# Optimization experiments

Hardware: AMD Instinct MI355X
Metric: run time of the kernel (lower is better)

Reference implementation:

```python
import jax, jax.numpy as jnp
import numpy as np

N_NODES = 100000; N_EDGES = 1600000; B = 16
IN_CH = 32; HID = 32; H1 = 4; OUT_CH = 32; H2 = 4; EDGE_DIM = 16
GMM_HID = 128; NUM_MIX = 3; ACTION_DIM = 10
NEG_SLOPE = 0.2  # PyG GATv2Conv default negative_slope


def _glorot(key, shape):
    return jax.random.normal(key, shape, dtype=jnp.float32) * (1.0 / np.sqrt(shape[-1]))


def setup_inputs() -> dict:
    key = jax.random.key(0)
    ks = jax.random.split(key, 20)
    x = jax.random.normal(ks[0], (N_NODES, IN_CH), jnp.float32)
    edge_index = jax.random.randint(ks[1], (2, N_EDGES), 0, N_NODES, dtype=jnp.int64)
    edge_attr = jax.random.normal(ks[2], (N_EDGES, EDGE_DIM), jnp.float32)
    batch = jnp.sort(jax.random.randint(ks[3], (N_NODES,), 0, B, dtype=jnp.int64))
    d1 = H1 * HID; d2 = H2 * OUT_CH
    return dict(
        x=x, edge_index=edge_index, edge_attr=edge_attr, batch=batch,
        W1l=_glorot(ks[4], (d1, IN_CH)), b1l=jnp.zeros((d1,), jnp.float32),
        W1r=_glorot(ks[5], (d1, IN_CH)), b1r=jnp.zeros((d1,), jnp.float32),
        W1e=_glorot(ks[6], (d1, EDGE_DIM)), att1=_glorot(ks[7], (H1, HID)),
        bias1=jnp.zeros((d1,), jnp.float32),
        W2l=_glorot(ks[8], (d2, d1)), b2l=jnp.zeros((d2,), jnp.float32),
        W2r=_glorot(ks[9], (d2, d1)), b2r=jnp.zeros((d2,), jnp.float32),
        W2e=_glorot(ks[10], (d2, EDGE_DIM)), att2=_glorot(ks[11], (H2, OUT_CH)),
        bias2=jnp.zeros((d2,), jnp.float32),
        Wg1=_glorot(ks[12], (GMM_HID, d2)), bg1=jnp.zeros((GMM_HID,), jnp.float32),
        Wg2=_glorot(ks[13], (NUM_MIX * 5, GMM_HID)), bg2=jnp.zeros((NUM_MIX * 5,), jnp.float32),
        Wp=_glorot(ks[14], (ACTION_DIM, d2)), bp=jnp.zeros((ACTION_DIM,), jnp.float32),
    )


def _gatv2(x, src, dst, ea, Wl, bl, Wr, br, We, att, bias, heads, ch):
    """PyG GATv2Conv with edge_dim, concat=True, add_self_loops=True (fill='mean'), eval mode."""
    N = x.shape[0]
    E = ea.shape[0]
    # self-loop edge_attr = mean of incoming edge attrs per target node (fill_value='mean')
    attr_sum = jax.ops.segment_sum(ea, dst, num_segments=N)
    cnt = jax.ops.segment_sum(jnp.ones((E, 1), ea.dtype), dst, num_segments=N)
    loop_attr = attr_sum / jnp.maximum(cnt, 1.0)
    loop = jnp.arange(N, dtype=src.dtype)
    s = jnp.concatenate([src, loop])
    d = jnp.concatenate([dst, loop])
    eaf = jnp.concatenate([ea, loop_attr], axis=0)  # [E+N, edge_dim]
    xl = (x @ Wl.T + bl).reshape(N, heads, ch)  # source transform (messages)
    xr = (x @ Wr.T + br).reshape(N, heads, ch)  # target transform
    ee = (eaf @ We.T).reshape(-1, heads, ch)
    m = jax.nn.leaky_relu(xl[s] + xr[d] + ee, NEG_SLOPE)  # [E+N, H, C]
    logit = jnp.einsum('ehc,hc->eh', m, att)  # attention logits per edge/head
    # segment softmax over edges sharing a target node (every node has a self-loop)
    mx = jax.ops.segment_max(logit, d, num_segments=N)
    ex = jnp.exp(logit - mx[d])
    den = jax.ops.segment_sum(ex, d, num_segments=N)
    alpha = ex / den[d]
    out = jax.ops.segment_sum(alpha[..., None] * xl[s], d, num_segments=N)  # [N, H, C]
    return out.reshape(N, heads * ch) + bias


def reference(x, edge_index, edge_attr, batch,
              W1l, b1l, W1r, b1r, W1e, att1, bias1,
              W2l, b2l, W2r, b2r, W2e, att2, bias2,
              Wg1, bg1, Wg2, bg2, Wp, bp):
    src, dst = edge_index[0], edge_index[1]
    y = jax.nn.elu(_gatv2(x, src, dst, edge_attr, W1l, b1l, W1r, b1r, W1e, att1, bias1, H1, HID))
    # dropout is identity in eval mode
    y = _gatv2(y, src, dst, edge_attr, W2l, b2l, W2r, b2r, W2e, att2, bias2, H2, OUT_CH)
    # global_mean_pool over batch
    gsum = jax.ops.segment_sum(y, batch, num_segments=B)
    gcnt = jax.ops.segment_sum(jnp.ones((y.shape[0], 1), y.dtype), batch, num_segments=B)
    g = gsum / jnp.maximum(gcnt, 1.0)  # [B, H2*OUT_CH]
    gmm_params = jax.nn.relu(g @ Wg1.T + bg1) @ Wg2.T + bg2  # [B, 15]
    num_proposals_logits = g @ Wp.T + bp  # [B, 10]
    return jnp.concatenate([gmm_params, num_proposals_logits], axis=-1)  # [B, 25]
```

## Files before the change

### kernel.cpp

```cpp
#include <hip/hip_runtime.h>
#include <math.h>

#define N_NODES 100000
#define N_EDGES 1600000
#define EN_TOT  (N_EDGES + N_NODES)
#define BATCH   16
#define EDGE_DIM 16
#define NEG_SLOPE 0.2f
#define NB_SCAN 391
#define LOG2E 1.44269504f

typedef float v2f __attribute__((ext_vector_type(2)));

__device__ __forceinline__ int rfl(int v) { return __builtin_amdgcn_readfirstlane(v); }

__device__ __forceinline__ v2f fma2(v2f a, v2f b, v2f c) {
#if __has_builtin(__builtin_elementwise_fma)
    return __builtin_elementwise_fma(a, b, c);
#else
    v2f r; r.x = fmaf(a.x, b.x, c.x); r.y = fmaf(a.y, b.y, c.y); return r;
#endif
}

template<int CTRL>
__device__ __forceinline__ float dpp_add(float p) {
    int t = __builtin_amdgcn_update_dpp(0, __float_as_int(p), CTRL, 0xF, 0xF, true);
    return p + __int_as_float(t);
}
__device__ __forceinline__ float red16(float p) {
    p = dpp_add<0xB1>(p);
    p = dpp_add<0x4E>(p);
    p = dpp_add<0x141>(p);
    p = dpp_add<0x140>(p);
    return p;
}

__global__ void zero_kernel(float* __restrict__ p, long long n) {
    long long i = (long long)blockIdx.x * blockDim.x + threadIdx.x;
    long long stride = (long long)gridDim.x * blockDim.x;
    for (; i < n; i += stride) p[i] = 0.0f;
}

__global__ void count_deg(const int* __restrict__ dst, int* __restrict__ deg,
                          int* __restrict__ rank) {
    int e = blockIdx.x * 256 + threadIdx.x;
    if (e < N_EDGES) rank[e] = atomicAdd(&deg[dst[e]], 1);
}

__global__ __launch_bounds__(256) void scan1(const int* __restrict__ deg,
                                             int* __restrict__ incl, int* __restrict__ bsum) {
    __shared__ int s[256];
    int n = blockIdx.x * 256 + threadIdx.x;
    int v = (n < N_NODES) ? deg[n] + 1 : 0;
    s[threadIdx.x] = v;
    __syncthreads();
    for (int off = 1; off < 256; off <<= 1) {
        int t = (threadIdx.x >= off) ? s[threadIdx.x - off] : 0;
        __syncthreads();
        s[threadIdx.x] += t;
        __syncthreads();
    }
    if (n < N_NODES) incl[n] = s[threadIdx.x];
    if (threadIdx.x == 255) bsum[blockIdx.x] = s[255];
}

__global__ __launch_bounds__(512) void scan2(int* __restrict__ bsum) {
    __shared__ int s[512];
    int t = threadIdx.x;
    int v = (t < NB_SCAN) ? bsum[t] : 0;
    s[t] = v;
    __syncthreads();
    for (int off = 1; off < 512; off <<= 1) {
        int u = (t >= off) ? s[t - off] : 0;
        __syncthreads();
        s[t] += u;
        __syncthreads();
    }
    if (t < NB_SCAN) bsum[t] = s[t] - v;
}

__global__ void scan3(const int* __restrict__ incl, const int* __restrict__ deg,
                      const int* __restrict__ bsum, int* __restrict__ offs) {
    int n = blockIdx.x * 256 + threadIdx.x;
    if (n < N_NODES) offs[n] = incl[n] - (deg[n] + 1) + bsum[blockIdx.x];
    if (n == 0) offs[N_NODES] = EN_TOT;
}

__global__ void scatter(const int* __restrict__ src, const int* __restrict__ dst,
                        const int* __restrict__ offs, const int* __restrict__ rank,
                        int2* __restrict__ csr) {
    int e = blockIdx.x * 256 + threadIdx.x;
    if (e < N_EDGES) {
        csr[offs[dst[e]] + rank[e]] = make_int2(src[e], e);
    } else if (e < EN_TOT) {
        int n = e - N_EDGES;
        csr[offs[n + 1] - 1] = make_int2(n, N_EDGES + n);
    }
}

__global__ __launch_bounds__(256) void loopattr_csr(const int* __restrict__ offs,
                                                    const int2* __restrict__ csr,
                                                    const float* __restrict__ ea,
                                                    float* __restrict__ lattr) {
    int node = blockIdx.x * 4 + (threadIdx.x >> 6);
    if (node >= N_NODES) return;
    int lane = threadIdx.x & 63;
    int row = offs[node];
    int degn = offs[node + 1] - 1 - row;
    int k = lane & 15, grp = lane >> 4;
    float acc = 0.0f;
    for (int i = grp; i < degn; i += 4) {
        int eid = csr[row + i].y;
        acc += ea[(long long)eid * EDGE_DIM + k];
    }
    acc += __shfl_xor(acc, 16);
    acc += __shfl_xor(acc, 32);
    if (lane < 16) lattr[(long long)node * EDGE_DIM + k] = acc / fmaxf((float)degn, 1.0f);
}

template<int K>
__global__ __launch_bounds__(256) void dual_linear(
    const float* __restrict__ in,
    const float* __restrict__ Wl, const float* __restrict__ bl,
    const float* __restrict__ Wr, const float* __restrict__ br,
    float* __restrict__ outl, float* __restrict__ outr, int N)
{
    constexpr int ROWS = 32;
    constexpr int K4 = K / 4;
    __shared__ float4 srow[ROWS][K4];
    int t = threadIdx.x;
    int base = blockIdx.x * ROWS;
    {
        const float4* in4 = (const float4*)in;
        for (int i = t; i < ROWS * K4; i += 256) {
            int r = i / K4, k = i - r * K4;
            int n = base + r;
            srow[r][k] = (n < N) ? in4[(size_t)n * K4 + k] : make_float4(0.f, 0.f, 0.f, 0.f);
        }
    }
    __syncthreads();
    const float* W  = (t < 128) ? Wl : Wr;
    const float* bb = (t < 128) ? bl : br;
    float* outp     = (t < 128) ? outl : outr;
    int j = t & 127;
    float bj = bb[j];
    float acc[ROWS];
#pragma unroll
    for (int r = 0; r < ROWS; ++r) acc[r] = bj;
    const float4* W4 = (const float4*)(W + (size_t)j * K);
    for (int kk = 0; kk < K4; ++kk) {
        float4 w = W4[kk];
#pragma unroll
        for (int r = 0; r < ROWS; ++r) {
            float4 a = srow[r][kk];
            acc[r] = fmaf(a.x, w.x, acc[r]);
            acc[r] = fmaf(a.y, w.y, acc[r]);
            acc[r] = fmaf(a.z, w.z, acc[r]);
            acc[r] = fmaf(a.w, w.w, acc[r]);
        }
    }
    for (int r = 0; r < ROWS; ++r) {
        int n = base + r;
        if (n < N) outp[(long long)n * 128 + j] = acc[r];
    }
}

template<int DO_ELU>
__global__ __launch_bounds__(256) void gat_fused(
    const int* __restrict__ offs, const int2* __restrict__ csr,
    const float* __restrict__ ea, const float* __restrict__ lattr,
    const float* __restrict__ We, const float* __restrict__ att,
    const v2f* __restrict__ xl2, const v2f* __restrict__ xr2,
    const float* __restrict__ bias, float* __restrict__ y)
{
    int node = blockIdx.x * 4 + (threadIdx.x >> 6);
    if (node >= N_NODES) return;
    int lane = threadIdx.x & 63;
    int c = lane << 1;

    v2f we0[8], we1[8];
    {
        const v2f* Wa = (const v2f*)(We + (size_t)c * EDGE_DIM);
        const v2f* Wb = (const v2f*)(We + (size_t)(c + 1) * EDGE_DIM);
#pragma unroll
        for (int q = 0; q < 8; ++q) { we0[q] = Wa[q]; we1[q] = Wb[q]; }
    }
    float2 atv = ((const float2*)att)[lane];
    float att0 = atv.x * LOG2E, att1 = atv.y * LOG2E;
    const float THR = 8.0f * LOG2E;

    int row  = rfl(offs[node]);
    int rend = rfl(offs[node + 1]);
    int last = rend - 1;
    v2f xrv = xr2[(size_t)node * 64 + lane];

    float m = -INFINITY, d = 0.f, acc0 = 0.f, acc1 = 0.f;

    auto attr_ptr = [&](int eid) -> const float4* {
        return (const float4*)((eid < N_EDGES) ? ea + (size_t)eid * EDGE_DIM
                                               : lattr + (size_t)(eid - N_EDGES) * EDGE_DIM);
    };

    auto body = [&](float4 A0, float4 A1, float4 A2, float4 A3, v2f xls) {
        v2f a[8] = { {A0.x,A0.y},{A0.z,A0.w},{A1.x,A1.y},{A1.z,A1.w},
                     {A2.x,A2.y},{A2.z,A2.w},{A3.x,A3.y},{A3.z,A3.w} };
        v2f ee0 = {0.f,0.f}, ee1 = {0.f,0.f};
#pragma unroll
        for (int q = 0; q < 8; ++q) {
            ee0 = fma2(a[q], we0[q], ee0);
            ee1 = fma2(a[q], we1[q], ee1);
        }
        float v0 = xls.x + xrv.x + ee0.x + ee0.y;
        float v1 = xls.y + xrv.y + ee1.x + ee1.y;
        v0 = fmaxf(v0, NEG_SLOPE * v0);
        v1 = fmaxf(v1, NEG_SLOPE * v1);
        float pl = red16(fmaf(v0, att0, v1 * att1));
        if (pl - m > THR) { float r_ = exp2f(m - pl); d *= r_; acc0 *= r_; acc1 *= r_; m = pl; }
        float w = exp2f(pl - m);
        d += w;
        acc0 = fmaf(w, xls.x, acc0);
        acc1 = fmaf(w, xls.y, acc1);
    };

    int2 se_a = csr[row];
    int2 se_b = csr[min(row + 1, last)];
    int2 se_c = csr[min(row + 2, last)];
    int2 se_d = csr[min(row + 3, last)];

    const float4* apA = attr_ptr(se_a.y);
    float4 Aa0 = apA[0], Aa1 = apA[1], Aa2 = apA[2], Aa3 = apA[3];
    v2f xlA = xl2[(size_t)se_a.x * 64 + lane];
    const float4* apB = attr_ptr(se_b.y);
    float4 Ab0 = apB[0], Ab1 = apB[1], Ab2 = apB[2], Ab3 = apB[3];
    v2f xlB = xl2[(size_t)se_b.x * 64 + lane];

    int i = row;
    for (; i + 1 < rend; i += 2) {
        body(Aa0, Aa1, Aa2, Aa3, xlA);
        {
            xlA = xl2[(size_t)se_c.x * 64 + lane];
            const float4* ap = attr_ptr(se_c.y);
            Aa0 = ap[0]; Aa1 = ap[1]; Aa2 = ap[2]; Aa3 = ap[3];
            se_c = csr[min(i + 4, last)];
        }
        body(Ab0, Ab1, Ab2, Ab3, xlB);
        {
            xlB = xl2[(size_t)se_d.x * 64 + lane];
            const float4* ap = attr_ptr(se_d.y);
            Ab0 = ap[0]; Ab1 = ap[1]; Ab2 = ap[2]; Ab3 = ap[3];
            se_d = csr[min(i + 5, last)];
        }
    }
    if (i < rend) body(Aa0, Aa1, Aa2, Aa3, xlA);

    float2 bv = ((const float2*)bias)[lane];
    float o0 = acc0 / d + bv.x;
    float o1 = acc1 / d + bv.y;
    if (DO_ELU) {
        o0 = (o0 > 0.0f) ? o0 : (__expf(o0) - 1.0f);
        o1 = (o1 > 0.0f) ? o1 : (__expf(o1) - 1.0f);
    }
    *(float2*)(y + (size_t)node * 128 + c) = make_float2(o0, o1);
}

__global__ __launch_bounds__(256) void pool_csr(const float* __restrict__ y,
                                                const int* __restrict__ batch,
                                                float* __restrict__ gsum,
                                                float* __restrict__ gcnt) {
    int base = blockIdx.x * 256;
    int t = threadIdx.x;
    int c = t & 127, h = t >> 7;
    int n = base + h;
    int end = min(base + 256, N_NODES);
    if (n >= end) return;
    float acc = 0.0f, cnt = 0.0f;
    int curb = batch[n];
    for (; n < end; n += 2) {
        int b = batch[n];
        if (b != curb) {
            atomicAdd(&gsum[curb * 128 + c], acc);
            if (c == 0) atomicAdd(&gcnt[curb], cnt);
            acc = 0.0f; cnt = 0.0f; curb = b;
        }
        acc += y[(long long)n * 128 + c];
        cnt += 1.0f;
    }
    atomicAdd(&gsum[curb * 128 + c], acc);
    if (c == 0) atomicAdd(&gcnt[curb], cnt);
}

__global__ __launch_bounds__(128) void head_kernel(
    const float* __restrict__ gsum, const float* __restrict__ gcnt,
    const float* __restrict__ Wg1, const float* __restrict__ bg1,
    const float* __restrict__ Wg2, const float* __restrict__ bg2,
    const float* __restrict__ Wp, const float* __restrict__ bp,
    float* __restrict__ out)
{
    int b = blockIdx.x;
    int j = threadIdx.x;
    __shared__ float g[128], h[128];
    float cntv = fmaxf(gcnt[b], 1.0f);
    g[j] = gsum[b * 128 + j] / cntv;
    __syncthreads();
    float a = bg1[j];
    for (int k = 0; k < 128; ++k) a += g[k] * Wg1[j * 128 + k];
    h[j] = fmaxf(a, 0.0f);
    __syncthreads();
    if (j < 15) {
        float o = bg2[j];
        for (int k = 0; k < 128; ++k) o += h[k] * Wg2[j * 128 + k];
        out[b * 25 + j] = o;
    }
    if (j >= 64 && j < 74) {
        int p = j - 64;
        float o = bp[p];
        for (int k = 0; k < 128; ++k) o += g[k] * Wp[p * 128 + k];
        out[b * 25 + 15 + p] = o;
    }
}

extern "C" void kernel_launch(void* const* d_in, const int* in_sizes, int n_in,
                              void* d_out, int out_size, void* d_ws, size_t ws_size,
                              hipStream_t stream)
{
    const float* x     = (const float*)d_in[0];
    const int*   ei    = (const int*)  d_in[1];
    const float* ea    = (const float*)d_in[2];
    const int*   batch = (const int*)  d_in[3];
    const float* W1l = (const float*)d_in[4],  *b1l  = (const float*)d_in[5];
    const float* W1r = (const float*)d_in[6],  *b1r  = (const float*)d_in[7];
    const float* W1e = (const float*)d_in[8],  *att1 = (const float*)d_in[9];
    const float* bias1 = (const float*)d_in[10];
    const float* W2l = (const float*)d_in[11], *b2l  = (const float*)d_in[12];
    const float* W2r = (const float*)d_in[13], *b2r  = (const float*)d_in[14];
    const float* W2e = (const float*)d_in[15], *att2 = (const float*)d_in[16];
    const float* bias2 = (const float*)d_in[17];
    const float* Wg1 = (const float*)d_in[18], *bg1 = (const float*)d_in[19];
    const float* Wg2 = (const float*)d_in[20], *bg2 = (const float*)d_in[21];
    const float* Wp  = (const float*)d_in[22], *bp  = (const float*)d_in[23];
    const int* src = ei;
    const int* dst = ei + N_EDGES;

    float* ws = (float*)d_ws;
    size_t o = 0;
    float* xl    = ws + o; o += (size_t)N_NODES * 128;
    float* xr    = ws + o; o += (size_t)N_NODES * 128;
    float* y     = ws + o; o += (size_t)N_NODES * 128;
    float* lattr = ws + o; o += (size_t)N_NODES * EDGE_DIM;
    int2* csr    = (int2*)(ws + o); o += (size_t)EN_TOT * 2;
    int* offs    = (int*)(ws + o); o += (size_t)N_NODES + 2;
    int* rank    = (int*)(ws + o); o += (size_t)N_EDGES;
    int* deg     = (int*)(ws + o); o += (size_t)N_NODES;
    float* gsum  = ws + o; o += (size_t)BATCH * 128;
    float* gcnt  = ws + o; o += (size_t)BATCH;
    int* bsum    = (int*)(ws + o); o += 512;
    int* incl    = (int*)y;

    float* out = (float*)d_out;

    long long nz = (long long)N_NODES + BATCH * 128 + BATCH;
    zero_kernel<<<512, 256, 0, stream>>>((float*)deg, nz);

    count_deg<<<(N_EDGES + 255) / 256, 256, 0, stream>>>(dst, deg, rank);
    scan1<<<NB_SCAN, 256, 0, stream>>>(deg, incl, bsum);
    scan2<<<1, 512, 0, stream>>>(bsum);
    scan3<<<NB_SCAN, 256, 0, stream>>>(incl, deg, bsum, offs);
    scatter<<<(EN_TOT + 255) / 256, 256, 0, stream>>>(src, dst, offs, rank, csr);
    loopattr_csr<<<(N_NODES + 3) / 4, 256, 0, stream>>>(offs, csr, ea, lattr);

    const int GAT_BLK = (N_NODES + 3) / 4;
    const int DL_BLK  = (N_NODES + 31) / 32;

    dual_linear<32><<<DL_BLK, 256, 0, stream>>>(x, W1l, b1l, W1r, b1r, xl, xr, N_NODES);
    gat_fused<1><<<GAT_BLK, 256, 0, stream>>>(offs, csr, ea, lattr,
                                              W1e, att1, (const v2f*)xl, (const v2f*)xr, bias1, y);

    dual_linear<128><<<DL_BLK, 256, 0, stream>>>(y, W2l, b2l, W2r, b2r, xl, xr, N_NODES);
    gat_fused<0><<<GAT_BLK, 256, 0, stream>>>(offs, csr, ea, lattr,
                                              W2e, att2, (const v2f*)xl, (const v2f*)xr, bias2, y);

    pool_csr<<<(N_NODES + 255) / 256, 256, 0, stream>>>(y, batch, gsum, gcnt);
    head_kernel<<<BATCH, 128, 0, stream>>>(gsum, gcnt, Wg1, bg1, Wg2, bg2, Wp, bp, out);
}
```

Measured before the change: 816.0 us.

## Derive self-loop edge embedding from mean of projected edge features in-kernel

Removes the separate loop-attribute kernel and lattr buffer. Because the edge projection is linear, the self-loop term is formed by averaging the projected edge embeddings accumulated during the neighbor loop. The self-loop edge is then processed after the loop using the node's own xl row. This avoids a CSR gather pass and per-edge branch selection between ea and lattr, at the cost of extra vector adds per edge in both GAT layers.

```diff
diff --git a/kernel.cpp b/kernel.cpp
--- a/kernel.cpp
+++ b/kernel.cpp
@@ -92,30 +92,7 @@
     int e = blockIdx.x * 256 + threadIdx.x;
     if (e < N_EDGES) {
         csr[offs[dst[e]] + rank[e]] = make_int2(src[e], e);
-    } else if (e < EN_TOT) {
-        int n = e - N_EDGES;
-        csr[offs[n + 1] - 1] = make_int2(n, N_EDGES + n);
-    }
-}
-
-__global__ __launch_bounds__(256) void loopattr_csr(const int* __restrict__ offs,
-                                                    const int2* __restrict__ csr,
-                                                    const float* __restrict__ ea,
-                                                    float* __restrict__ lattr) {
-    int node = blockIdx.x * 4 + (threadIdx.x >> 6);
-    if (node >= N_NODES) return;
-    int lane = threadIdx.x & 63;
-    int row = offs[node];
-    int degn = offs[node + 1] - 1 - row;
-    int k = lane & 15, grp = lane >> 4;
-    float acc = 0.0f;
-    for (int i = grp; i < degn; i += 4) {
-        int eid = csr[row + i].y;
-        acc += ea[(long long)eid * EDGE_DIM + k];
-    }
-    acc += __shfl_xor(acc, 16);
-    acc += __shfl_xor(acc, 32);
-    if (lane < 16) lattr[(long long)node * EDGE_DIM + k] = acc / fmaxf((float)degn, 1.0f);
+    }
 }
 
 template<int K>
@@ -168,7 +145,7 @@
 template<int DO_ELU>
 __global__ __launch_bounds__(256) void gat_fused(
     const int* __restrict__ offs, const int2* __restrict__ csr,
-    const float* __restrict__ ea, const float* __restrict__ lattr,
+    const float* __restrict__ ea,
     const float* __restrict__ We, const float* __restrict__ att,
     const v2f* __restrict__ xl2, const v2f* __restrict__ xr2,
     const float* __restrict__ bias, float* __restrict__ y)
@@ -191,15 +168,12 @@
 
     int row  = rfl(offs[node]);
     int rend = rfl(offs[node + 1]);
-    int last = rend - 1;
+    int degn  = rend - 1 - row;
+    int rlast = rend - 2;
     v2f xrv = xr2[(size_t)node * 64 + lane];
 
     float m = -INFINITY, d = 0.f, acc0 = 0.f, acc1 = 0.f;
-
-    auto attr_ptr = [&](int eid) -> const float4* {
-        return (const float4*)((eid < N_EDGES) ? ea + (size_t)eid * EDGE_DIM
-                                               : lattr + (size_t)(eid - N_EDGES) * EDGE_DIM);
-    };
+    v2f eesum0 = {0.f, 0.f}, eesum1 = {0.f, 0.f};
 
     auto body = [&](float4 A0, float4 A1, float4 A2, float4 A3, v2f xls) {
         v2f a[8] = { {A0.x,A0.y},{A0.z,A0.w},{A1.x,A1.y},{A1.z,A1.w},
@@ -210,6 +184,8 @@
             ee0 = fma2(a[q], we0[q], ee0);
             ee1 = fma2(a[q], we1[q], ee1);
         }
+        eesum0 += ee0;
+        eesum1 += ee1;
         float v0 = xls.x + xrv.x + ee0.x + ee0.y;
         float v1 = xls.y + xrv.y + ee1.x + ee1.y;
         v0 = fmaxf(v0, NEG_SLOPE * v0);
@@ -222,36 +198,55 @@
         acc1 = fmaf(w, xls.y, acc1);
     };
 
-    int2 se_a = csr[row];
-    int2 se_b = csr[min(row + 1, last)];
-    int2 se_c = csr[min(row + 2, last)];
-    int2 se_d = csr[min(row + 3, last)];
-
-    const float4* apA = attr_ptr(se_a.y);
-    float4 Aa0 = apA[0], Aa1 = apA[1], Aa2 = apA[2], Aa3 = apA[3];
-    v2f xlA = xl2[(size_t)se_a.x * 64 + lane];
-    const float4* apB = attr_ptr(se_b.y);
-    float4 Ab0 = apB[0], Ab1 = apB[1], Ab2 = apB[2], Ab3 = apB[3];
-    v2f xlB = xl2[(size_t)se_b.x * 64 + lane];
-
-    int i = row;
-    for (; i + 1 < rend; i += 2) {
-        body(Aa0, Aa1, Aa2, Aa3, xlA);
-        {
-            xlA = xl2[(size_t)se_c.x * 64 + lane];
-            const float4* ap = attr_ptr(se_c.y);
-            Aa0 = ap[0]; Aa1 = ap[1]; Aa2 = ap[2]; Aa3 = ap[3];
-            se_c = csr[min(i + 4, last)];
-        }
-        body(Ab0, Ab1, Ab2, Ab3, xlB);
-        {
-            xlB = xl2[(size_t)se_d.x * 64 + lane];
-            const float4* ap = attr_ptr(se_d.y);
-            Ab0 = ap[0]; Ab1 = ap[1]; Ab2 = ap[2]; Ab3 = ap[3];
-            se_d = csr[min(i + 5, last)];
-        }
-    }
-    if (i < rend) body(Aa0, Aa1, Aa2, Aa3, xlA);
+    if (degn > 0) {
+        int2 se_a = csr[row];
+        int2 se_b = csr[min(row + 1, rlast)];
+        int2 se_c = csr[min(row + 2, rlast)];
+        int2 se_d = csr[min(row + 3, rlast)];
+
+        const float4* apA = (const float4*)(ea + (size_t)se_a.y * EDGE_DIM);
+        float4 Aa0 = apA[0], Aa1 = apA[1], Aa2 = apA[2], Aa3 = apA[3];
+        v2f xlA = xl2[(size_t)se_a.x * 64 + lane];
+        const float4* apB = (const float4*)(ea + (size_t)se_b.y * EDGE_DIM);
+        float4 Ab0 = apB[0], Ab1 = apB[1], Ab2 = apB[2], Ab3 = apB[3];
+        v2f xlB = xl2[(size_t)se_b.x * 64 + lane];
+
+        int i = row;
+        for (; i + 1 < rend - 1; i += 2) {
+            body(Aa0, Aa1, Aa2, Aa3, xlA);
+            {
+                xlA = xl2[(size_t)se_c.x * 64 + lane];
+                const float4* ap = (const float4*)(ea + (size_t)se_c.y * EDGE_DIM);
+                Aa0 = ap[0]; Aa1 = ap[1]; Aa2 = ap[2]; Aa3 = ap[3];
+                se_c = csr[min(i + 4, rlast)];
+            }
+            body(Ab0, Ab1, Ab2, Ab3, xlB);
+            {
+                xlB = xl2[(size_t)se_d.x * 64 + lane];
+                const float4* ap = (const float4*)(ea + (size_t)se_d.y * EDGE_DIM);
+                Ab0 = ap[0]; Ab1 = ap[1]; Ab2 = ap[2]; Ab3 = ap[3];
+                se_d = csr[min(i + 5, rlast)];
+            }
+        }
+        if (i < rend - 1) body(Aa0, Aa1, Aa2, Aa3, xlA);
+    }
+
+    {
+        float inv = (degn > 0) ? 1.0f / (float)degn : 0.0f;
+        v2f ee0 = eesum0 * (v2f){inv, inv};
+        v2f ee1 = eesum1 * (v2f){inv, inv};
+        v2f xls = xl2[(size_t)node * 64 + lane];
+        float v0 = xls.x + xrv.x + ee0.x + ee0.y;
+        float v1 = xls.y + xrv.y + ee1.x + ee1.y;
+        v0 = fmaxf(v0, NEG_SLOPE * v0);
+        v1 = fmaxf(v1, NEG_SLOPE * v1);
+        float pl = red16(fmaf(v0, att0, v1 * att1));
+        if (pl - m > THR) { float r_ = exp2f(m - pl); d *= r_; acc0 *= r_; acc1 *= r_; m = pl; }
+        float w = exp2f(pl - m);
+        d += w;
+        acc0 = fmaf(w, xls.x, acc0);
+        acc1 = fmaf(w, xls.y, acc1);
+    }
 
     float2 bv = ((const float2*)bias)[lane];
     float o0 = acc0 / d + bv.x;
@@ -346,7 +341,6 @@
     float* xl    = ws + o; o += (size_t)N_NODES * 128;
     float* xr    = ws + o; o += (size_t)N_NODES * 128;
     float* y     = ws + o; o += (size_t)N_NODES * 128;
-    float* lattr = ws + o; o += (size_t)N_NODES * EDGE_DIM;
     int2* csr    = (int2*)(ws + o); o += (size_t)EN_TOT * 2;
     int* offs    = (int*)(ws + o); o += (size_t)N_NODES + 2;
     int* rank    = (int*)(ws + o); o += (size_t)N_EDGES;
@@ -365,18 +359,17 @@
     scan1<<<NB_SCAN, 256, 0, stream>>>(deg, incl, bsum);
     scan2<<<1, 512, 0, stream>>>(bsum);
     scan3<<<NB_SCAN, 256, 0, stream>>>(incl, deg, bsum, offs);
-    scatter<<<(EN_TOT + 255) / 256, 256, 0, stream>>>(src, dst, offs, rank, csr);
-    loopattr_csr<<<(N_NODES + 3) / 4, 256, 0, stream>>>(offs, csr, ea, lattr);
+    scatter<<<(N_EDGES + 255) / 256, 256, 0, stream>>>(src, dst, offs, rank, csr);
 
     const int GAT_BLK = (N_NODES + 3) / 4;
     const int DL_BLK  = (N_NODES + 31) / 32;
 
     dual_linear<32><<<DL_BLK, 256, 0, stream>>>(x, W1l, b1l, W1r, b1r, xl, xr, N_NODES);
-    gat_fused<1><<<GAT_BLK, 256, 0, stream>>>(offs, csr, ea, lattr,
+    gat_fused<1><<<GAT_BLK, 256, 0, stream>>>(offs, csr, ea,
                                               W1e, att1, (const v2f*)xl, (const v2f*)xr, bias1, y);
 
     dual_linear<128><<<DL_BLK, 256, 0, stream>>>(y, W2l, b2l, W2r, b2r, xl, xr, N_NODES);
-    gat_fused<0><<<GAT_BLK, 256, 0, stream>>>(offs, csr, ea, lattr,
+    gat_fused<0><<<GAT_BLK, 256, 0, stream>>>(offs, csr, ea,
                                               W2e, att2, (const v2f*)xl, (const v2f*)xr, bias2, y);
 
     pool_csr<<<(N_NODES + 255) / 256, 256, 0, stream>>>(y, batch, gsum, gcnt);
```

After: 778.9 us. 1.05x faster.
